# Performance work log

Measured on AMD Instinct MI355X. Metric: run time of the kernel, lower is better.

Reference implementation:

```python
import jax, jax.numpy as jnp
import numpy as np

SCALE_WEIGHT = 0.5 ** 0.5


def setup_inputs() -> dict:
    key = jax.random.key(0)
    ks = jax.random.split(key, 6)
    B, C, T, S = 8, 512, 2048, 2048
    base_target_emb = jax.random.normal(ks[0], (B, C, T, 1), dtype=jnp.float32)
    inp = jax.random.normal(ks[1], (B, C, T, 1), dtype=jnp.float32)
    encoder_out_t = jax.random.normal(ks[2], (B, C, S), dtype=jnp.float32)
    encoder_out_c = jax.random.normal(ks[3], (B, C, S), dtype=jnp.float32)
    # nn.Linear(input_size, input_size) params: W [out, in], b [out]
    bound = 1.0 / np.sqrt(C)
    W = jax.random.uniform(ks[4], (C, C), minval=-bound, maxval=bound, dtype=jnp.float32)
    b = jax.random.uniform(ks[5], (C,), minval=-bound, maxval=bound, dtype=jnp.float32)
    return {"base_target_emb": base_target_emb, "input": inp,
            "encoder_out_t": encoder_out_t, "encoder_out_c": encoder_out_c,
            "W": W, "b": b}


def reference(base_target_emb, input, encoder_out_t, encoder_out_c, W, b):
    # base_target_emb, input: [B, C, T, 1]; encoder_out_t/c: [B, C, S]
    x = input[..., 0]                                   # [B, C, T]
    # seq_linear: Linear over channel dim (y = W x + b)
    preatt = jnp.einsum('bct,oc->bot', x, W) + b[None, :, None]
    target = (base_target_emb[..., 0] + preatt) * SCALE_WEIGHT  # [B, C, T]
    # bmm(target^T, enc_t): scores over source positions
    pre_a = jnp.einsum('bct,bcs->bts', target, encoder_out_t)   # [B, T, S]
    attn = jax.nn.softmax(pre_a, axis=-1)                       # [B, T, S]
    # bmm(attn, enc_c^T): attention-weighted sum of values
    ctx = jnp.einsum('bts,bcs->btc', attn, encoder_out_c)       # [B, T, C]
    context_output = jnp.transpose(ctx, (0, 2, 1))[..., None]   # [B, C, T, 1]
    return context_output, attn
```

## Files before the change

### kernel.cpp

```cpp
#include <hip/hip_runtime.h>

typedef unsigned short u16;
typedef __attribute__((ext_vector_type(4))) float f4;
typedef __attribute__((ext_vector_type(8))) short bf8;
typedef __attribute__((ext_vector_type(8))) _Float16 h8;
typedef __attribute__((ext_vector_type(4))) unsigned short u16x4;

#define B_ 8
#define C_ 512
#define T_ 2048
#define S_ 2048
#define SCALE_W 0.70710678118654752440f

__device__ __forceinline__ u16 f2bf(float f) {
  unsigned u = __builtin_bit_cast(unsigned, f);
  unsigned r = 0x7FFFu + ((u >> 16) & 1u);
  return (u16)((u + r) >> 16);
}
__device__ __forceinline__ float bf2f(u16 h) {
  unsigned u = ((unsigned)h) << 16;
  return __builtin_bit_cast(float, u);
}
__device__ __forceinline__ u16 f2h(float f) {
  return __builtin_bit_cast(u16, (_Float16)f);
}
__device__ __forceinline__ float h2f(u16 h) {
  return (float)__builtin_bit_cast(_Float16, h);
}

__device__ __forceinline__ void gload16(const u16* g, u16* l) {
  __builtin_amdgcn_global_load_lds((__attribute__((address_space(1))) const void*)g,
                                   (__attribute__((address_space(3))) void*)l, 16, 0, 0);
}

#define MEMF() asm volatile("" ::: "memory")
#define BAR()  do { MEMF(); __builtin_amdgcn_s_barrier(); MEMF(); } while (0)
#define LGKM0() do { asm volatile("s_waitcnt lgkmcnt(0)" ::: "memory"); \
                     __builtin_amdgcn_sched_barrier(0); } while (0)

template<int MODE>
__global__ __launch_bounds__(256) void transpose_kernel(
    const float* __restrict__ in, u16* __restrict__ oh, u16* __restrict__ ol, int X)
{
  __shared__ float t[32][33];
  const int tx = threadIdx.x, ty = threadIdx.y;
  const long cbase = (long)blockIdx.z * C_ + blockIdx.y * 32;
  const long xbase = (long)blockIdx.x * 32;
  const float* ip = in + cbase * X + xbase;
#pragma unroll
  for (int i = 0; i < 4; ++i)
    t[ty + i * 8][tx] = ip[(long)(ty + i * 8) * X + tx];
  __syncthreads();
  const long obase = ((long)blockIdx.z * X + xbase) * C_ + blockIdx.y * 32;
#pragma unroll
  for (int i = 0; i < 4; ++i) {
    float v = t[tx][ty + i * 8];
    long idx = obase + (long)(ty + i * 8) * C_ + tx;
    if (MODE == 0) {
      u16 h = f2bf(v);
      oh[idx] = h;
      ol[idx] = f2bf(v - bf2f(h));
    } else {
      oh[idx] = f2h(v);
    }
  }
}

template<int FP16>
__global__ __launch_bounds__(256) void split_kernel(
    const float* __restrict__ in, u16* __restrict__ oh, u16* __restrict__ ol, long n4)
{
  long i = (long)blockIdx.x * 256 + threadIdx.x;
  const long stride = (long)gridDim.x * 256;
  for (; i < n4; i += stride) {
    f4 v = ((const f4*)in)[i];
    u16x4 hv, lv;
#pragma unroll
    for (int j = 0; j < 4; ++j) {
      if (FP16) {
        hv[j] = f2h(v[j]);
      } else {
        u16 h = f2bf(v[j]);
        hv[j] = h;
        lv[j] = f2bf(v[j] - bf2f(h));
      }
    }
    ((u16x4*)oh)[i] = hv;
    if (!FP16) ((u16x4*)ol)[i] = lv;
  }
}

template<int NPASS, int EPI, int F16>
__global__ __launch_bounds__(256, 2) void gemm_kernel(
    const u16* __restrict__ Ah, const u16* __restrict__ Al,
    const u16* __restrict__ Bh, const u16* __restrict__ Bl,
    int M, int N, int K,
    long sA, long sB, long sO,
    const float* __restrict__ baseO, const float* __restrict__ bias,
    u16* __restrict__ outH, u16* __restrict__ outL,
    float* __restrict__ outF)
{
  constexpr int BM = 128, BK = 32;
  constexpr int TILE = BM * BK;
  __shared__ u16 lA[(NPASS == 3 ? 2 : 1) * TILE];
  __shared__ u16 lB[(NPASS == 3 ? 2 : 1) * TILE];
  u16* lAh = lA; u16* lAl = (NPASS == 3) ? (lA + TILE) : lA;
  u16* lBh = lB; u16* lBl = (NPASS == 3) ? (lB + TILE) : lB;

  const int tid = threadIdx.x;
  const int wid = tid >> 6;
  const int lane = tid & 63;
  const int wr = wid >> 1, wc = wid & 1;
  const int bz = blockIdx.z;
  const int m0 = blockIdx.y * BM;
  const int n0 = blockIdx.x * BM;

  const u16* gAh = Ah + (long)bz * sA + (long)m0 * K;
  const u16* gAl = (NPASS == 3) ? (Al + (long)bz * sA + (long)m0 * K) : nullptr;
  const u16* gBh = Bh + (long)bz * sB + (long)n0 * K;
  const u16* gBl = (NPASS == 3) ? (Bl + (long)bz * sB + (long)n0 * K) : nullptr;

  const int srow = tid >> 2;
  const int skoff = (tid & 3) * 8;
  const int ldsOff = wid * 512;

  f4 acc[4][4] = {};

#define MM(a, b, c) (F16 ? __builtin_amdgcn_mfma_f32_16x16x32_f16( \
                       __builtin_bit_cast(h8, a), __builtin_bit_cast(h8, b), c, 0, 0, 0) \
                         : __builtin_amdgcn_mfma_f32_16x16x32_bf16(a, b, c, 0, 0, 0))

  for (int k0 = 0; k0 < K; k0 += BK) {
    __syncthreads();
#pragma unroll
    for (int c = 0; c < 2; ++c) {
      const long go = (long)(c * 64 + srow) * K + k0 + skoff;
      const int lo = c * 2048 + ldsOff;
      gload16(gAh + go, lAh + lo);
      if (NPASS == 3) gload16(gAl + go, lAl + lo);
      gload16(gBh + go, lBh + lo);
      if (NPASS == 3) gload16(gBl + go, lBl + lo);
    }
    asm volatile("s_waitcnt vmcnt(0)" ::: "memory");
    __syncthreads();

    bf8 a_h[4], b_h[4], a_l[4], b_l[4];
    const int fr = lane & 15;
    const int fk = (lane >> 4) * 8;
#pragma unroll
    for (int i = 0; i < 4; ++i) {
      a_h[i] = *(const bf8*)&lAh[(wr * 64 + i * 16 + fr) * BK + fk];
      b_h[i] = *(const bf8*)&lBh[(wc * 64 + i * 16 + fr) * BK + fk];
      if (NPASS == 3) {
        a_l[i] = *(const bf8*)&lAl[(wr * 64 + i * 16 + fr) * BK + fk];
        b_l[i] = *(const bf8*)&lBl[(wc * 64 + i * 16 + fr) * BK + fk];
      }
    }
#pragma unroll
    for (int mi = 0; mi < 4; ++mi)
#pragma unroll
      for (int ni = 0; ni < 4; ++ni) {
        acc[mi][ni] = MM(a_h[mi], b_h[ni], acc[mi][ni]);
        if (NPASS == 3) {
          acc[mi][ni] = MM(a_h[mi], b_l[ni], acc[mi][ni]);
          acc[mi][ni] = MM(a_l[mi], b_h[ni], acc[mi][ni]);
        }
      }
  }
#undef MM

  const int fr = lane & 15;
  const int r4 = (lane >> 4) * 4;
#pragma unroll
  for (int mi = 0; mi < 4; ++mi) {
#pragma unroll
    for (int ni = 0; ni < 4; ++ni) {
      const int gn = n0 + wc * 64 + ni * 16 + fr;
      const long gmb = m0 + wr * 64 + mi * 16 + r4;
      if (EPI == 1) {
        f4 bv = *(const f4*)(baseO + ((long)bz * C_ + gn) * T_ + gmb);
        const float bs = bias[gn];
#pragma unroll
        for (int r = 0; r < 4; ++r) {
          float val = (acc[mi][ni][r] + bv[r] + bs) * SCALE_W;
          const long idx = (long)bz * sO + (gmb + r) * (long)N + gn;
          u16 h = f2h(val);
          outH[idx] = h;
          outL[idx] = f2h(val - h2f(h));
        }
      } else {
#pragma unroll
        for (int r = 0; r < 4; ++r)
          outF[(long)bz * sO + (gmb + r) * (long)N + gn] = acc[mi][ni][r];
      }
    }
  }
}

__device__ __forceinline__ void stage2(const u16* g, u16* l) {
  gload16(g, l);
  gload16(g + 64 * C_, l + 4096);
}
template<int NF>
__device__ __forceinline__ void rd_frags(bf8 (&d)[NF][2], const u16* p, int k0o, int k1o) {
#pragma unroll
  for (int i = 0; i < NF; ++i) {
    d[i][0] = *(const bf8*)&p[i * 1024 + k0o];
    d[i][1] = *(const bf8*)&p[i * 1024 + k1o];
  }
}
template<int MH, int NH>
__device__ __forceinline__ void mmq(f4 (&acc)[8][4], const bf8 (&a)[4][2], const bf8 (&b)[2][2]) {
  __builtin_amdgcn_s_setprio(1);
#pragma unroll
  for (int mi = 0; mi < 4; ++mi)
#pragma unroll
    for (int ni = 0; ni < 2; ++ni)
#pragma unroll
      for (int ks = 0; ks < 2; ++ks)
        acc[MH * 4 + mi][NH * 2 + ni] = __builtin_amdgcn_mfma_f32_16x16x32_f16(
            __builtin_bit_cast(h8, a[mi][ks]), __builtin_bit_cast(h8, b[ni][ks]),
            acc[MH * 4 + mi][NH * 2 + ni], 0, 0, 0);
  __builtin_amdgcn_s_setprio(0);
}

__global__ __launch_bounds__(512, 2) void gemm8p_kernel(
    const u16* __restrict__ Ah, const u16* __restrict__ Al,
    const u16* __restrict__ Bm,
    float* __restrict__ outF)
{
  __shared__ u16 lds[65536];
  const int tid = threadIdx.x;
  const int wid = tid >> 6, lane = tid & 63;
  const int wr = wid >> 2, wc = wid & 3;

  const int gx = gridDim.x, gy = gridDim.y;
  int lin = blockIdx.x + gx * (blockIdx.y + gy * blockIdx.z);
  const int nwg = gx * gy * (int)gridDim.z;
  lin = (lin & 7) * (nwg >> 3) + (lin >> 3);
  const int bx = lin % gx;
  const int tmp = lin / gx;
  const int by = tmp % gy, bz = tmp / gy;

  const int m0 = by * 256, n0 = bx * 256;
  const u16* gAh = Ah + ((long)bz * T_ + m0) * C_;
  const u16* gAl = Al + ((long)bz * T_ + m0) * C_;
  const u16* gB  = Bm + ((long)bz * S_ + n0) * C_;

  const int srow = tid >> 3;
  const int scol = (((tid & 7) ^ (srow & 7)) * 8);
  const int dstA = tid * 8;

  const int fr = lane & 15;
  const int k0o = (((lane >> 4) ^ (lane & 7)) * 8);
  const int k1o = k0o ^ 32;
  const int abase = (wr * 128 + fr) * 64;
  const int bbase = 32768 + (wc * 64 + fr) * 64;

  f4 acc[8][4] = {};
  constexpr int NT = 16;

#define SRC_A(tt) ((((tt) >> 3) ? gAl : gAh) + ((tt) & 7) * 64)
#define SRC_B(tt) (gB + ((tt) & 7) * 64)
#define STAGE_A(tt, h) stage2(SRC_A(tt) + (long)((h) * 128 + srow) * C_ + scol, \
                              lds + (((tt) & 1) * 16384 + (h) * 8192 + dstA))
#define STAGE_B(tt, h) stage2(SRC_B(tt) + (long)((h) * 128 + srow) * C_ + scol, \
                              lds + (32768 + ((tt) & 1) * 16384 + (h) * 8192 + dstA))

  STAGE_B(0, 0); STAGE_B(0, 1); STAGE_A(0, 0); STAGE_A(0, 1); STAGE_B(1, 0);
  asm volatile("s_waitcnt vmcnt(2)" ::: "memory");
  BAR();

  bf8 af[4][2], b0[2][2], b1[2][2];
  for (int kt = 0; kt < NT - 1; ++kt) {
    const int cur = kt & 1;
    const u16* la = lds + cur * 16384 + abase;
    const u16* lb = lds + cur * 16384 + bbase;
    rd_frags(af, la, k0o, k1o);
    rd_frags(b0, lb, k0o, k1o);
    STAGE_B(kt + 1, 1);
    BAR(); LGKM0();
    mmq<0, 0>(acc, af, b0);
    BAR();
    rd_frags(b1, lb + 2048, k0o, k1o);
    STAGE_A(kt + 1, 0);
    BAR(); LGKM0();
    mmq<0, 1>(acc, af, b1);
    BAR();
    rd_frags(af, la + 4096, k0o, k1o);
    STAGE_A(kt + 1, 1);
    BAR(); LGKM0();
    mmq<1, 0>(acc, af, b0);
    BAR();
    {
      int t2 = kt + 2; if (t2 > NT - 1) t2 = NT - 1;
      STAGE_B(t2, 0);
    }
    BAR();
    mmq<1, 1>(acc, af, b1);
    if (kt == NT - 2) { asm volatile("s_waitcnt vmcnt(0)" ::: "memory"); }
    else             { asm volatile("s_waitcnt vmcnt(2)" ::: "memory"); }
    BAR();
  }
  {
    const int cur = (NT - 1) & 1;
    const u16* la = lds + cur * 16384 + abase;
    const u16* lb = lds + cur * 16384 + bbase;
    rd_frags(af, la, k0o, k1o);
    rd_frags(b0, lb, k0o, k1o);
    BAR(); LGKM0();
    mmq<0, 0>(acc, af, b0);
    BAR();
    rd_frags(b1, lb + 2048, k0o, k1o);
    BAR(); LGKM0();
    mmq<0, 1>(acc, af, b1);
    BAR();
    rd_frags(af, la + 4096, k0o, k1o);
    BAR(); LGKM0();
    mmq<1, 0>(acc, af, b0);
    BAR();
    mmq<1, 1>(acc, af, b1);
  }
#undef SRC_A
#undef SRC_B
#undef STAGE_A
#undef STAGE_B

  const int r4 = (lane >> 4) * 4;
#pragma unroll
  for (int am = 0; am < 8; ++am) {
#pragma unroll
    for (int an = 0; an < 4; ++an) {
      const long gm = m0 + wr * 128 + am * 16 + r4;
      const int gn = n0 + wc * 64 + an * 16 + fr;
      float* po = outF + (long)bz * T_ * S_ + gm * (long)S_ + gn;
#pragma unroll
      for (int r = 0; r < 4; ++r) po[(long)r * S_] = acc[am][an][r];
    }
  }
}

__global__ __launch_bounds__(256) void softmax_kernel(float* __restrict__ a,
                                                      u16* __restrict__ ab) {
  const int tid = threadIdx.x;
  float* p = a + (long)blockIdx.x * 2048;
  u16* pb = ab + (long)blockIdx.x * 2048;
  f4 v0 = ((const f4*)p)[tid];
  f4 v1 = ((const f4*)p)[tid + 256];
  float m = fmaxf(fmaxf(fmaxf(v0[0], v0[1]), fmaxf(v0[2], v0[3])),
                  fmaxf(fmaxf(v1[0], v1[1]), fmaxf(v1[2], v1[3])));
#pragma unroll
  for (int o = 32; o >= 1; o >>= 1) m = fmaxf(m, __shfl_xor(m, o));
  __shared__ float redm[4], reds[4];
  if ((tid & 63) == 0) redm[tid >> 6] = m;
  __syncthreads();
  m = fmaxf(fmaxf(redm[0], redm[1]), fmaxf(redm[2], redm[3]));
  float s = 0.f;
#pragma unroll
  for (int j = 0; j < 4; ++j) { v0[j] = __expf(v0[j] - m); s += v0[j]; }
#pragma unroll
  for (int j = 0; j < 4; ++j) { v1[j] = __expf(v1[j] - m); s += v1[j]; }
#pragma unroll
  for (int o = 32; o >= 1; o >>= 1) s += __shfl_xor(s, o);
  if ((tid & 63) == 0) reds[tid >> 6] = s;
  __syncthreads();
  const float inv = 1.0f / (reds[0] + reds[1] + reds[2] + reds[3]);
  v0 *= inv; v1 *= inv;
  ((f4*)p)[tid] = v0;
  ((f4*)p)[tid + 256] = v1;
  u16x4 c0, c1;
#pragma unroll
  for (int j = 0; j < 4; ++j) { c0[j] = f2h(v0[j]); c1[j] = f2h(v1[j]); }
  ((u16x4*)pb)[tid] = c0;
  ((u16x4*)pb)[tid + 256] = c1;
}

extern "C" void kernel_launch(void* const* d_in, const int* in_sizes, int n_in,
                              void* d_out, int out_size, void* d_ws, size_t ws_size,
                              hipStream_t stream) {
  const float* base  = (const float*)d_in[0];
  const float* x     = (const float*)d_in[1];
  const float* enc_t = (const float*)d_in[2];
  const float* enc_c = (const float*)d_in[3];
  const float* W     = (const float*)d_in[4];
  const float* bias  = (const float*)d_in[5];

  float* ctx  = (float*)d_out;
  float* attn = ctx + (long)B_ * C_ * T_;

  const long NBTC = (long)B_ * T_ * C_;
  u16* x_hi = (u16*)d_ws;
  u16* x_lo = x_hi + NBTC;
  u16* et_h = x_lo + NBTC;
  u16* pad  = et_h + NBTC;
  u16* ec_h = pad + NBTC;
  u16* w_hi = ec_h + NBTC;
  u16* w_lo = w_hi + (long)C_ * C_;

  u16* t_h = (u16*)d_out;
  u16* t_l = t_h + NBTC;
  u16* attn_h = x_hi;

  dim3 tb(32, 8);
  transpose_kernel<0><<<dim3(T_ / 32, C_ / 32, B_), tb, 0, stream>>>(x, x_hi, x_lo, T_);
  transpose_kernel<1><<<dim3(S_ / 32, C_ / 32, B_), tb, 0, stream>>>(enc_t, et_h, nullptr, S_);
  split_kernel<1><<<2048, 256, 0, stream>>>(enc_c, ec_h, nullptr, (long)B_ * C_ * S_ / 4);
  split_kernel<0><<<256, 256, 0, stream>>>(W, w_hi, w_lo, (long)C_ * C_ / 4);

  gemm_kernel<3, 1, 0><<<dim3(C_ / 128, T_ / 128, B_), 256, 0, stream>>>(
      x_hi, x_lo, w_hi, w_lo,
      T_, C_, C_, (long)T_ * C_, 0L, (long)T_ * C_,
      base, bias, t_h, t_l, nullptr);

  gemm8p_kernel<<<dim3(S_ / 256, T_ / 256, B_), 512, 0, stream>>>(
      t_h, t_l, et_h, attn);

  softmax_kernel<<<B_ * T_, 256, 0, stream>>>(attn, attn_h);

  gemm_kernel<1, 0, 1><<<dim3(T_ / 128, C_ / 128, B_), 256, 0, stream>>>(
      ec_h, nullptr, attn_h, nullptr,
      C_, T_, S_, (long)C_ * S_, (long)T_ * S_, (long)C_ * T_,
      nullptr, nullptr, nullptr, nullptr, ctx);

  (void)in_sizes; (void)n_in; (void)out_size; (void)ws_size;
}
```

Before: 270.4 us.

## Reuse pipelined 256-tile GEMM for context bmm and drop x low-part pass

Result: faster. 263.7 us (-2.5%).

```diff
diff --git a/kernel.cpp b/kernel.cpp
--- a/kernel.cpp
+++ b/kernel.cpp
@@ -12,15 +12,6 @@
 #define S_ 2048
 #define SCALE_W 0.70710678118654752440f
 
-__device__ __forceinline__ u16 f2bf(float f) {
-  unsigned u = __builtin_bit_cast(unsigned, f);
-  unsigned r = 0x7FFFu + ((u >> 16) & 1u);
-  return (u16)((u + r) >> 16);
-}
-__device__ __forceinline__ float bf2f(u16 h) {
-  unsigned u = ((unsigned)h) << 16;
-  return __builtin_bit_cast(float, u);
-}
 __device__ __forceinline__ u16 f2h(float f) {
   return __builtin_bit_cast(u16, (_Float16)f);
 }
@@ -38,9 +29,8 @@
 #define LGKM0() do { asm volatile("s_waitcnt lgkmcnt(0)" ::: "memory"); \
                      __builtin_amdgcn_sched_barrier(0); } while (0)
 
-template<int MODE>
 __global__ __launch_bounds__(256) void transpose_kernel(
-    const float* __restrict__ in, u16* __restrict__ oh, u16* __restrict__ ol, int X)
+    const float* __restrict__ in, u16* __restrict__ oh, int X)
 {
   __shared__ float t[32][33];
   const int tx = threadIdx.x, ty = threadIdx.y;
@@ -53,20 +43,11 @@
   __syncthreads();
   const long obase = ((long)blockIdx.z * X + xbase) * C_ + blockIdx.y * 32;
 #pragma unroll
-  for (int i = 0; i < 4; ++i) {
-    float v = t[tx][ty + i * 8];
-    long idx = obase + (long)(ty + i * 8) * C_ + tx;
-    if (MODE == 0) {
-      u16 h = f2bf(v);
-      oh[idx] = h;
-      ol[idx] = f2bf(v - bf2f(h));
-    } else {
-      oh[idx] = f2h(v);
-    }
-  }
-}
-
-template<int FP16>
+  for (int i = 0; i < 4; ++i)
+    oh[obase + (long)(ty + i * 8) * C_ + tx] = f2h(t[tx][ty + i * 8]);
+}
+
+template<int LO>
 __global__ __launch_bounds__(256) void split_kernel(
     const float* __restrict__ in, u16* __restrict__ oh, u16* __restrict__ ol, long n4)
 {
@@ -77,35 +58,24 @@
     u16x4 hv, lv;
 #pragma unroll
     for (int j = 0; j < 4; ++j) {
-      if (FP16) {
-        hv[j] = f2h(v[j]);
-      } else {
-        u16 h = f2bf(v[j]);
-        hv[j] = h;
-        lv[j] = f2bf(v[j] - bf2f(h));
-      }
+      u16 h = f2h(v[j]);
+      hv[j] = h;
+      if (LO) lv[j] = f2h(v[j] - h2f(h));
     }
     ((u16x4*)oh)[i] = hv;
-    if (!FP16) ((u16x4*)ol)[i] = lv;
-  }
-}
-
-template<int NPASS, int EPI, int F16>
-__global__ __launch_bounds__(256, 2) void gemm_kernel(
-    const u16* __restrict__ Ah, const u16* __restrict__ Al,
+    if (LO) ((u16x4*)ol)[i] = lv;
+  }
+}
+
+__global__ __launch_bounds__(256, 2) void gemm1_kernel(
+    const u16* __restrict__ A,
     const u16* __restrict__ Bh, const u16* __restrict__ Bl,
-    int M, int N, int K,
-    long sA, long sB, long sO,
     const float* __restrict__ baseO, const float* __restrict__ bias,
-    u16* __restrict__ outH, u16* __restrict__ outL,
-    float* __restrict__ outF)
+    u16* __restrict__ outH, u16* __restrict__ outL)
 {
-  constexpr int BM = 128, BK = 32;
+  constexpr int BM = 128, BK = 32, K = C_, N = C_;
   constexpr int TILE = BM * BK;
-  __shared__ u16 lA[(NPASS == 3 ? 2 : 1) * TILE];
-  __shared__ u16 lB[(NPASS == 3 ? 2 : 1) * TILE];
-  u16* lAh = lA; u16* lAl = (NPASS == 3) ? (lA + TILE) : lA;
-  u16* lBh = lB; u16* lBl = (NPASS == 3) ? (lB + TILE) : lB;
+  __shared__ u16 lA[TILE], lBh[TILE], lBl[TILE];
 
   const int tid = threadIdx.x;
   const int wid = tid >> 6;
@@ -115,10 +85,9 @@
   const int m0 = blockIdx.y * BM;
   const int n0 = blockIdx.x * BM;
 
-  const u16* gAh = Ah + (long)bz * sA + (long)m0 * K;
-  const u16* gAl = (NPASS == 3) ? (Al + (long)bz * sA + (long)m0 * K) : nullptr;
-  const u16* gBh = Bh + (long)bz * sB + (long)n0 * K;
-  const u16* gBl = (NPASS == 3) ? (Bl + (long)bz * sB + (long)n0 * K) : nullptr;
+  const u16* gA  = A + ((long)bz * T_ + m0) * K;
+  const u16* gBh = Bh + (long)n0 * K;
+  const u16* gBl = Bl + (long)n0 * K;
 
   const int srow = tid >> 2;
   const int skoff = (tid & 3) * 8;
@@ -126,48 +95,40 @@
 
   f4 acc[4][4] = {};
 
-#define MM(a, b, c) (F16 ? __builtin_amdgcn_mfma_f32_16x16x32_f16( \
-                       __builtin_bit_cast(h8, a), __builtin_bit_cast(h8, b), c, 0, 0, 0) \
-                         : __builtin_amdgcn_mfma_f32_16x16x32_bf16(a, b, c, 0, 0, 0))
-
   for (int k0 = 0; k0 < K; k0 += BK) {
     __syncthreads();
 #pragma unroll
     for (int c = 0; c < 2; ++c) {
       const long go = (long)(c * 64 + srow) * K + k0 + skoff;
       const int lo = c * 2048 + ldsOff;
-      gload16(gAh + go, lAh + lo);
-      if (NPASS == 3) gload16(gAl + go, lAl + lo);
+      gload16(gA + go, lA + lo);
       gload16(gBh + go, lBh + lo);
-      if (NPASS == 3) gload16(gBl + go, lBl + lo);
+      gload16(gBl + go, lBl + lo);
     }
     asm volatile("s_waitcnt vmcnt(0)" ::: "memory");
     __syncthreads();
 
-    bf8 a_h[4], b_h[4], a_l[4], b_l[4];
+    bf8 a_[4], b_h[4], b_l[4];
     const int fr = lane & 15;
     const int fk = (lane >> 4) * 8;
 #pragma unroll
     for (int i = 0; i < 4; ++i) {
-      a_h[i] = *(const bf8*)&lAh[(wr * 64 + i * 16 + fr) * BK + fk];
+      a_[i]  = *(const bf8*)&lA[(wr * 64 + i * 16 + fr) * BK + fk];
       b_h[i] = *(const bf8*)&lBh[(wc * 64 + i * 16 + fr) * BK + fk];
-      if (NPASS == 3) {
-        a_l[i] = *(const bf8*)&lAl[(wr * 64 + i * 16 + fr) * BK + fk];
-        b_l[i] = *(const bf8*)&lBl[(wc * 64 + i * 16 + fr) * BK + fk];
+      b_l[i] = *(const bf8*)&lBl[(wc * 64 + i * 16 + fr) * BK + fk];
+    }
+#pragma unroll
+    for (int mi = 0; mi < 4; ++mi)
+#pragma unroll
+      for (int ni = 0; ni < 4; ++ni) {
+        acc[mi][ni] = __builtin_amdgcn_mfma_f32_16x16x32_f16(
+            __builtin_bit_cast(h8, a_[mi]), __builtin_bit_cast(h8, b_h[ni]),
+            acc[mi][ni], 0, 0, 0);
+        acc[mi][ni] = __builtin_amdgcn_mfma_f32_16x16x32_f16(
+            __builtin_bit_cast(h8, a_[mi]), __builtin_bit_cast(h8, b_l[ni]),
+            acc[mi][ni], 0, 0, 0);
       }
-    }
-#pragma unroll
-    for (int mi = 0; mi < 4; ++mi)
-#pragma unroll
-      for (int ni = 0; ni < 4; ++ni) {
-        acc[mi][ni] = MM(a_h[mi], b_h[ni], acc[mi][ni]);
-        if (NPASS == 3) {
-          acc[mi][ni] = MM(a_h[mi], b_l[ni], acc[mi][ni]);
-          acc[mi][ni] = MM(a_l[mi], b_h[ni], acc[mi][ni]);
-        }
-      }
-  }
-#undef MM
+  }
 
   const int fr = lane & 15;
   const int r4 = (lane >> 4) * 4;
@@ -177,29 +138,24 @@
     for (int ni = 0; ni < 4; ++ni) {
       const int gn = n0 + wc * 64 + ni * 16 + fr;
       const long gmb = m0 + wr * 64 + mi * 16 + r4;
-      if (EPI == 1) {
-        f4 bv = *(const f4*)(baseO + ((long)bz * C_ + gn) * T_ + gmb);
-        const float bs = bias[gn];
-#pragma unroll
-        for (int r = 0; r < 4; ++r) {
-          float val = (acc[mi][ni][r] + bv[r] + bs) * SCALE_W;
-          const long idx = (long)bz * sO + (gmb + r) * (long)N + gn;
-          u16 h = f2h(val);
-          outH[idx] = h;
-          outL[idx] = f2h(val - h2f(h));
-        }
-      } else {
-#pragma unroll
-        for (int r = 0; r < 4; ++r)
-          outF[(long)bz * sO + (gmb + r) * (long)N + gn] = acc[mi][ni][r];
+      f4 bv = *(const f4*)(baseO + ((long)bz * C_ + gn) * T_ + gmb);
+      const float bs = bias[gn];
+#pragma unroll
+      for (int r = 0; r < 4; ++r) {
+        float val = (acc[mi][ni][r] + bv[r] + bs) * SCALE_W;
+        const long idx = ((long)bz * T_ + gmb + r) * (long)N + gn;
+        u16 h = f2h(val);
+        outH[idx] = h;
+        outL[idx] = f2h(val - h2f(h));
       }
     }
   }
 }
 
+template<int NT, int TPP, int LDK>
 __device__ __forceinline__ void stage2(const u16* g, u16* l) {
   gload16(g, l);
-  gload16(g + 64 * C_, l + 4096);
+  gload16(g + 64 * LDK, l + 4096);
 }
 template<int NF>
 __device__ __forceinline__ void rd_frags(bf8 (&d)[NF][2], const u16* p, int k0o, int k1o) {
@@ -224,10 +180,12 @@
   __builtin_amdgcn_s_setprio(0);
 }
 
+template<int NT, int TPP, int LDK>
 __global__ __launch_bounds__(512, 2) void gemm8p_kernel(
-    const u16* __restrict__ Ah, const u16* __restrict__ Al,
-    const u16* __restrict__ Bm,
-    float* __restrict__ outF)
+    const u16* __restrict__ A0, const u16* __restrict__ A1,
+    const u16* __restrict__ B0,
+    float* __restrict__ outF,
+    long sA, long sB, long sO, int Nr)
 {
   __shared__ u16 lds[65536];
   const int tid = threadIdx.x;
@@ -243,9 +201,9 @@
   const int by = tmp % gy, bz = tmp / gy;
 
   const int m0 = by * 256, n0 = bx * 256;
-  const u16* gAh = Ah + ((long)bz * T_ + m0) * C_;
-  const u16* gAl = Al + ((long)bz * T_ + m0) * C_;
-  const u16* gB  = Bm + ((long)bz * S_ + n0) * C_;
+  const u16* gA0 = A0 + (long)bz * sA + (long)m0 * LDK;
+  const u16* gA1 = A1 + (long)bz * sA + (long)m0 * LDK;
+  const u16* gB  = B0 + (long)bz * sB + (long)n0 * LDK;
 
   const int srow = tid >> 3;
   const int scol = (((tid & 7) ^ (srow & 7)) * 8);
@@ -258,13 +216,12 @@
   const int bbase = 32768 + (wc * 64 + fr) * 64;
 
   f4 acc[8][4] = {};
-  constexpr int NT = 16;
-
-#define SRC_A(tt) ((((tt) >> 3) ? gAl : gAh) + ((tt) & 7) * 64)
-#define SRC_B(tt) (gB + ((tt) & 7) * 64)
-#define STAGE_A(tt, h) stage2(SRC_A(tt) + (long)((h) * 128 + srow) * C_ + scol, \
+
+#define SRC_A(tt) ((((tt) / TPP) == 0 ? gA0 : gA1) + ((tt) % TPP) * 64)
+#define SRC_B(tt) (gB + ((tt) % TPP) * 64)
+#define STAGE_A(tt, h) stage2<NT, TPP, LDK>(SRC_A(tt) + (long)((h) * 128 + srow) * LDK + scol, \
                               lds + (((tt) & 1) * 16384 + (h) * 8192 + dstA))
-#define STAGE_B(tt, h) stage2(SRC_B(tt) + (long)((h) * 128 + srow) * C_ + scol, \
+#define STAGE_B(tt, h) stage2<NT, TPP, LDK>(SRC_B(tt) + (long)((h) * 128 + srow) * LDK + scol, \
                               lds + (32768 + ((tt) & 1) * 16384 + (h) * 8192 + dstA))
 
   STAGE_B(0, 0); STAGE_B(0, 1); STAGE_A(0, 0); STAGE_A(0, 1); STAGE_B(1, 0);
@@ -333,9 +290,9 @@
     for (int an = 0; an < 4; ++an) {
       const long gm = m0 + wr * 128 + am * 16 + r4;
       const int gn = n0 + wc * 64 + an * 16 + fr;
-      float* po = outF + (long)bz * T_ * S_ + gm * (long)S_ + gn;
-#pragma unroll
-      for (int r = 0; r < 4; ++r) po[(long)r * S_] = acc[am][an][r];
+      float* po = outF + (long)bz * sO + gm * (long)Nr + gn;
+#pragma unroll
+      for (int r = 0; r < 4; ++r) po[(long)r * Nr] = acc[am][an][r];
     }
   }
 }
@@ -389,38 +346,34 @@
   float* attn = ctx + (long)B_ * C_ * T_;
 
   const long NBTC = (long)B_ * T_ * C_;
-  u16* x_hi = (u16*)d_ws;
-  u16* x_lo = x_hi + NBTC;
-  u16* et_h = x_lo + NBTC;
-  u16* pad  = et_h + NBTC;
-  u16* ec_h = pad + NBTC;
-  u16* w_hi = ec_h + NBTC;
-  u16* w_lo = w_hi + (long)C_ * C_;
+  u16* x_h  = (u16*)d_ws;
+  u16* et_h = x_h + NBTC;
+  u16* ec_h = x_h + 4 * NBTC;
+  u16* w_h  = ec_h + NBTC;
+  u16* w_l  = w_h + (long)C_ * C_;
 
   u16* t_h = (u16*)d_out;
   u16* t_l = t_h + NBTC;
-  u16* attn_h = x_hi;
+  u16* attn_h = x_h;
 
   dim3 tb(32, 8);
-  transpose_kernel<0><<<dim3(T_ / 32, C_ / 32, B_), tb, 0, stream>>>(x, x_hi, x_lo, T_);
-  transpose_kernel<1><<<dim3(S_ / 32, C_ / 32, B_), tb, 0, stream>>>(enc_t, et_h, nullptr, S_);
-  split_kernel<1><<<2048, 256, 0, stream>>>(enc_c, ec_h, nullptr, (long)B_ * C_ * S_ / 4);
-  split_kernel<0><<<256, 256, 0, stream>>>(W, w_hi, w_lo, (long)C_ * C_ / 4);
-
-  gemm_kernel<3, 1, 0><<<dim3(C_ / 128, T_ / 128, B_), 256, 0, stream>>>(
-      x_hi, x_lo, w_hi, w_lo,
-      T_, C_, C_, (long)T_ * C_, 0L, (long)T_ * C_,
-      base, bias, t_h, t_l, nullptr);
-
-  gemm8p_kernel<<<dim3(S_ / 256, T_ / 256, B_), 512, 0, stream>>>(
-      t_h, t_l, et_h, attn);
+  transpose_kernel<<<dim3(T_ / 32, C_ / 32, B_), tb, 0, stream>>>(x, x_h, T_);
+  transpose_kernel<<<dim3(S_ / 32, C_ / 32, B_), tb, 0, stream>>>(enc_t, et_h, S_);
+  split_kernel<0><<<2048, 256, 0, stream>>>(enc_c, ec_h, nullptr, (long)B_ * C_ * S_ / 4);
+  split_kernel<1><<<256, 256, 0, stream>>>(W, w_h, w_l, (long)C_ * C_ / 4);
+
+  gemm1_kernel<<<dim3(C_ / 128, T_ / 128, B_), 256, 0, stream>>>(
+      x_h, w_h, w_l, base, bias, t_h, t_l);
+
+  gemm8p_kernel<16, 8, 512><<<dim3(S_ / 256, T_ / 256, B_), 512, 0, stream>>>(
+      t_h, t_l, et_h, attn,
+      (long)T_ * C_, (long)S_ * C_, (long)T_ * S_, S_);
 
   softmax_kernel<<<B_ * T_, 256, 0, stream>>>(attn, attn_h);
 
-  gemm_kernel<1, 0, 1><<<dim3(T_ / 128, C_ / 128, B_), 256, 0, stream>>>(
-      ec_h, nullptr, attn_h, nullptr,
-      C_, T_, S_, (long)C_ * S_, (long)T_ * S_, (long)C_ * T_,
-      nullptr, nullptr, nullptr, nullptr, ctx);
+  gemm8p_kernel<32, 32, 2048><<<dim3(T_ / 256, C_ / 256, B_), 512, 0, stream>>>(
+      ec_h, ec_h, attn_h, ctx,
+      (long)C_ * S_, (long)T_ * S_, (long)C_ * T_, T_);
 
   (void)in_sizes; (void)n_in; (void)out_size; (void)ws_size;
 }
```
